# Optimization experiments

Hardware: AMD Instinct MI355X
Metric: run time of the kernel (lower is better)

## Reference

```python
import jax, jax.numpy as jnp
import numpy as np

H = 32  # hidden_size
I = 1   # input_size
O = 12  # fc output

def setup_inputs() -> dict:
    key = jax.random.key(0)
    ks = jax.random.split(key, 8)
    B, T = 4096, 512
    s_ih = 1.0 / np.sqrt(H)
    x = jax.random.normal(ks[0], (B, T, I), dtype=jnp.float32)
    w_ih = jax.random.uniform(ks[1], (3 * H, I), minval=-s_ih, maxval=s_ih, dtype=jnp.float32)
    w_hh = jax.random.uniform(ks[2], (3 * H, H), minval=-s_ih, maxval=s_ih, dtype=jnp.float32)
    b_ih = jax.random.uniform(ks[3], (3 * H,), minval=-s_ih, maxval=s_ih, dtype=jnp.float32)
    b_hh = jax.random.uniform(ks[4], (3 * H,), minval=-s_ih, maxval=s_ih, dtype=jnp.float32)
    s_fc = 1.0 / np.sqrt(H)
    fc_w = jax.random.uniform(ks[5], (O, H), minval=-s_fc, maxval=s_fc, dtype=jnp.float32)
    fc_b = jax.random.uniform(ks[6], (O,), minval=-s_fc, maxval=s_fc, dtype=jnp.float32)
    return {"x": x, "w_ih": w_ih, "w_hh": w_hh, "b_ih": b_ih, "b_hh": b_hh, "fc_w": fc_w, "fc_b": fc_b}

def _gru_last_hidden(x, w_ih, w_hh, b_ih, b_hh):
    # x: [B, T, I]. Precompute input projections for all timesteps: [B, T, 3H]
    gi = jnp.einsum('bti,gi->btg', x, w_ih) + b_ih
    gi = jnp.swapaxes(gi, 0, 1)  # [T, B, 3H] for scan over time
    B = x.shape[0]
    h0 = jnp.zeros((B, H), dtype=x.dtype)

    def step(h, gi_t):
        gh = h @ w_hh.T + b_hh  # [B, 3H]
        i_r, i_z, i_n = jnp.split(gi_t, 3, axis=-1)
        h_r, h_z, h_n = jnp.split(gh, 3, axis=-1)
        r = jax.nn.sigmoid(i_r + h_r)
        z = jax.nn.sigmoid(i_z + h_z)
        n = jnp.tanh(i_n + r * h_n)
        h_new = (1.0 - z) * n + z * h
        return h_new, None

    h_last, _ = jax.lax.scan(step, h0, gi)
    return h_last  # [B, H]

def reference(x, w_ih, w_hh, b_ih, b_hh, fc_w, fc_b):
    h_last = _gru_last_hidden(x, w_ih, w_hh, b_ih, b_hh)
    return h_last @ fc_w.T + fc_b  # [B, 12]
```

## Files before the change

### kernel.cpp

```cpp
#include <hip/hip_runtime.h>


namespace {

typedef _Float16 f16;
typedef _Float16 f16x8 __attribute__((ext_vector_type(8)));
typedef float    f32x4 __attribute__((ext_vector_type(4)));

constexpr int kT = 512;
constexpr float kL2E = 1.4426950408889634f;

__device__ __forceinline__ float fast_exp2(float a) {
#if __has_builtin(__builtin_amdgcn_exp2f)
    return __builtin_amdgcn_exp2f(a);
#else
    return exp2f(a);
#endif
}
__device__ __forceinline__ float fast_rcp(float a) {
#if __has_builtin(__builtin_amdgcn_rcpf)
    return __builtin_amdgcn_rcpf(a);
#else
    return 1.0f / a;
#endif
}

union B128 {
    int   w[4];
    f16x8 v;
};

__device__ __forceinline__ float sel4(const f32x4& a, bool b0, bool b1) {
    const float x01 = b0 ? a[1] : a[0];
    const float x23 = b0 ? a[3] : a[2];
    return b1 ? x23 : x01;
}

__global__ __launch_bounds__(64)
__attribute__((amdgpu_waves_per_eu(1, 1)))
void gru_k32s2(
    const float* __restrict__ x,
    const float* __restrict__ w_ih,
    const float* __restrict__ w_hh,
    const float* __restrict__ b_ih,
    const float* __restrict__ b_hh,
    const float* __restrict__ fc_w,
    const float* __restrict__ fc_b,
    float* __restrict__ out)
{
    __shared__ float hf[4 * 33];

    const int lane = threadIdx.x;
    const int c    = lane & 15;
    const int lg   = lane >> 4;
    const int q    = c >> 2;
    const int j    = c & 3;
    const int blk  = blockIdx.x;

    f16x8 wA[3][2];
#pragma unroll
    for (int g = 0; g < 3; ++g) {
        const float s = (g < 2) ? -kL2E : 2.0f * kL2E;
#pragma unroll
        for (int hh = 0; hh < 2; ++hh) {
            f16x8 f;
#pragma unroll
            for (int i = 0; i < 8; ++i) {
                const int k = ((i & 1) << 4) | (lg << 2) | (i >> 1);
                f[i] = (f16)(s * w_hh[(g * 32 + hh * 16 + c) * 32 + k]);
            }
            wA[g][hh] = f;
        }
    }

    f32x4 biasC[3][2];
#pragma unroll
    for (int hh = 0; hh < 2; ++hh)
#pragma unroll
        for (int v = 0; v < 4; ++v) {
            const int u = hh * 16 + 4 * lg + v;
            biasC[0][hh][v] = -kL2E * (b_ih[u] + b_hh[u]);
            biasC[1][hh][v] = -kL2E * (b_ih[u + 32] + b_hh[u + 32]);
            biasC[2][hh][v] = 2.0f * kL2E * b_hh[u + 64];
        }

    float cwr[2], cwz[2], cwn[2], cbn[2];
#pragma unroll
    for (int hh = 0; hh < 2; ++hh) {
        const int u = hh * 16 + 4 * lg + q;
        cwr[hh] = -kL2E * w_ih[u];
        cwz[hh] = -kL2E * w_ih[u + 32];
        cwn[hh] = 2.0f * kL2E * w_ih[u + 64];
        cbn[hh] = 2.0f * kL2E * b_ih[u + 64];
    }
    const bool b0 = (q & 1) != 0;
    const bool b1 = (q & 2) != 0;

    float hlo = 0.0f, hhi = 0.0f;
    B128 B;
    B.w[0] = 0; B.w[1] = 0; B.w[2] = 0; B.w[3] = 0;

    const float4* xrow = reinterpret_cast<const float4*>(
        x + ((size_t)blk * 4 + j) * kT);
    float4 xcur = xrow[0];

    for (int t0 = 0; t0 < kT; t0 += 4) {
        const int nq = (t0 + 4 < kT) ? (t0 >> 2) + 1 : (t0 >> 2);
        float4 xnext = xrow[nq];

#pragma unroll
        for (int tt = 0; tt < 4; ++tt) {
            const float xt = (tt == 0) ? xcur.x : (tt == 1) ? xcur.y
                           : (tt == 2) ? xcur.z : xcur.w;

            f32x4 aR[2], aZ[2], aN[2];
#pragma unroll
            for (int hh = 0; hh < 2; ++hh) {
                aR[hh] = __builtin_amdgcn_mfma_f32_16x16x32_f16(wA[0][hh], B.v, biasC[0][hh], 0, 0, 0);
                aZ[hh] = __builtin_amdgcn_mfma_f32_16x16x32_f16(wA[1][hh], B.v, biasC[1][hh], 0, 0, 0);
                aN[hh] = __builtin_amdgcn_mfma_f32_16x16x32_f16(wA[2][hh], B.v, biasC[2][hh], 0, 0, 0);
            }

#pragma unroll
            for (int hh = 0; hh < 2; ++hh) {
                const float pr = sel4(aR[hh], b0, b1);
                const float pz = sel4(aZ[hh], b0, b1);
                const float pn = sel4(aN[hh], b0, b1);
                const float ar  = fmaf(xt, cwr[hh], pr);
                const float az  = fmaf(xt, cwz[hh], pz);
                const float inn = fmaf(xt, cwn[hh], cbn[hh]);
                const float sr = 1.0f + fast_exp2(ar);
                const float sz = 1.0f + fast_exp2(az);
                const float ip = fast_rcp(sr * sz);
                const float r  = ip * sz;
                const float z  = ip * sr;
                const float n = fmaf(-2.0f,
                    fast_rcp(1.0f + fast_exp2(fmaf(r, pn, inn))), 1.0f);
                if (hh == 0) hlo = fmaf(z, hlo - n, n);
                else         hhi = fmaf(z, hhi - n, n);
            }

            const int pk = __builtin_bit_cast(int,
                __builtin_amdgcn_cvt_pkrtz(hlo, hhi));
            B.w[0] = __builtin_amdgcn_ds_swizzle(pk, 0x0013);
            B.w[1] = __builtin_amdgcn_ds_swizzle(pk, 0x0093);
            B.w[2] = __builtin_amdgcn_ds_swizzle(pk, 0x0113);
            B.w[3] = __builtin_amdgcn_ds_swizzle(pk, 0x0193);
        }
        xcur = xnext;
    }

    hf[j * 33 + 4 * lg + q]      = hlo;
    hf[j * 33 + 16 + 4 * lg + q] = hhi;
    __syncthreads();
    if (lane < 48) {
        const int row = lane / 12, o = lane % 12;
        float acc = fc_b[o];
#pragma unroll
        for (int k = 0; k < 32; ++k)
            acc = fmaf(fc_w[o * 32 + k], hf[row * 33 + k], acc);
        out[((size_t)blk * 4 + row) * 12 + o] = acc;
    }
}

}

extern "C" void kernel_launch(void* const* d_in, const int* in_sizes, int n_in,
                              void* d_out, int out_size, void* d_ws, size_t ws_size,
                              hipStream_t stream) {
    const float* x    = (const float*)d_in[0];
    const float* w_ih = (const float*)d_in[1];
    const float* w_hh = (const float*)d_in[2];
    const float* b_ih = (const float*)d_in[3];
    const float* b_hh = (const float*)d_in[4];
    const float* fc_w = (const float*)d_in[5];
    const float* fc_b = (const float*)d_in[6];
    float* out = (float*)d_out;

    dim3 grid(1024);
    dim3 block(64);
    gru_k32s2<<<grid, block, 0, stream>>>(x, w_ih, w_hh, b_ih, b_hh, fc_w, fc_b, out);
}
```

Before: 120.4 us.

## Split GRU hidden units across two waves with LDS exchange per step

Each block now runs two wavefronts, and each one owns 16 of the 32 hidden units, so a wave issues 3 MFMAs per step instead of 6. The new hidden state is exchanged through double-buffered shared memory with a __syncthreads every timestep, replacing the in-wave ds_swizzle broadcast. This is meant to halve the serial per-wave work on the recurrent critical path. In exchange it adds an LDS store, a block barrier and an LDS load to every one of the 512 dependent steps.

```diff
diff --git a/kernel.cpp b/kernel.cpp
--- a/kernel.cpp
+++ b/kernel.cpp
@@ -25,20 +25,15 @@
 #endif
 }
 
-union B128 {
-    int   w[4];
-    f16x8 v;
-};
-
 __device__ __forceinline__ float sel4(const f32x4& a, bool b0, bool b1) {
     const float x01 = b0 ? a[1] : a[0];
     const float x23 = b0 ? a[3] : a[2];
     return b1 ? x23 : x01;
 }
 
-__global__ __launch_bounds__(64)
-__attribute__((amdgpu_waves_per_eu(1, 1)))
-void gru_k32s2(
+__global__ __launch_bounds__(128)
+__attribute__((amdgpu_waves_per_eu(2, 2)))
+void gru_2w(
     const float* __restrict__ x,
     const float* __restrict__ w_ih,
     const float* __restrict__ w_hh,
@@ -48,57 +43,49 @@
     const float* __restrict__ fc_b,
     float* __restrict__ out)
 {
+    __shared__ f16   hbuf[2][4][32];
     __shared__ float hf[4 * 33];
 
-    const int lane = threadIdx.x;
+    const int tid  = threadIdx.x;
+    const int w    = tid >> 6;
+    const int lane = tid & 63;
     const int c    = lane & 15;
     const int lg   = lane >> 4;
     const int q    = c >> 2;
     const int j    = c & 3;
     const int blk  = blockIdx.x;
 
-    f16x8 wA[3][2];
+    f16x8 wA[3];
 #pragma unroll
     for (int g = 0; g < 3; ++g) {
         const float s = (g < 2) ? -kL2E : 2.0f * kL2E;
+        f16x8 f;
 #pragma unroll
-        for (int hh = 0; hh < 2; ++hh) {
-            f16x8 f;
-#pragma unroll
-            for (int i = 0; i < 8; ++i) {
-                const int k = ((i & 1) << 4) | (lg << 2) | (i >> 1);
-                f[i] = (f16)(s * w_hh[(g * 32 + hh * 16 + c) * 32 + k]);
-            }
-            wA[g][hh] = f;
-        }
+        for (int i = 0; i < 8; ++i)
+            f[i] = (f16)(s * w_hh[(g * 32 + w * 16 + c) * 32 + 8 * lg + i]);
+        wA[g] = f;
     }
 
-    f32x4 biasC[3][2];
+    f32x4 biasC[3];
 #pragma unroll
-    for (int hh = 0; hh < 2; ++hh)
-#pragma unroll
-        for (int v = 0; v < 4; ++v) {
-            const int u = hh * 16 + 4 * lg + v;
-            biasC[0][hh][v] = -kL2E * (b_ih[u] + b_hh[u]);
-            biasC[1][hh][v] = -kL2E * (b_ih[u + 32] + b_hh[u + 32]);
-            biasC[2][hh][v] = 2.0f * kL2E * b_hh[u + 64];
-        }
+    for (int v = 0; v < 4; ++v) {
+        const int u = w * 16 + 4 * lg + v;
+        biasC[0][v] = -kL2E * (b_ih[u] + b_hh[u]);
+        biasC[1][v] = -kL2E * (b_ih[u + 32] + b_hh[u + 32]);
+        biasC[2][v] = 2.0f * kL2E * b_hh[u + 64];
+    }
 
-    float cwr[2], cwz[2], cwn[2], cbn[2];
-#pragma unroll
-    for (int hh = 0; hh < 2; ++hh) {
-        const int u = hh * 16 + 4 * lg + q;
-        cwr[hh] = -kL2E * w_ih[u];
-        cwz[hh] = -kL2E * w_ih[u + 32];
-        cwn[hh] = 2.0f * kL2E * w_ih[u + 64];
-        cbn[hh] = 2.0f * kL2E * b_ih[u + 64];
-    }
+    const int u = w * 16 + 4 * lg + q;
+    const float cwr = -kL2E * w_ih[u];
+    const float cwz = -kL2E * w_ih[u + 32];
+    const float cwn = 2.0f * kL2E * w_ih[u + 64];
+    const float cbn = 2.0f * kL2E * b_ih[u + 64];
     const bool b0 = (q & 1) != 0;
     const bool b1 = (q & 2) != 0;
 
-    float hlo = 0.0f, hhi = 0.0f;
-    B128 B;
-    B.w[0] = 0; B.w[1] = 0; B.w[2] = 0; B.w[3] = 0;
+    float h = 0.0f;
+    f16x8 B = {(f16)0, (f16)0, (f16)0, (f16)0,
+               (f16)0, (f16)0, (f16)0, (f16)0};
 
     const float4* xrow = reinterpret_cast<const float4*>(
         x + ((size_t)blk * 4 + j) * kT);
@@ -112,49 +99,38 @@
         for (int tt = 0; tt < 4; ++tt) {
             const float xt = (tt == 0) ? xcur.x : (tt == 1) ? xcur.y
                            : (tt == 2) ? xcur.z : xcur.w;
+            const int buf = tt & 1;
 
-            f32x4 aR[2], aZ[2], aN[2];
-#pragma unroll
-            for (int hh = 0; hh < 2; ++hh) {
-                aR[hh] = __builtin_amdgcn_mfma_f32_16x16x32_f16(wA[0][hh], B.v, biasC[0][hh], 0, 0, 0);
-                aZ[hh] = __builtin_amdgcn_mfma_f32_16x16x32_f16(wA[1][hh], B.v, biasC[1][hh], 0, 0, 0);
-                aN[hh] = __builtin_amdgcn_mfma_f32_16x16x32_f16(wA[2][hh], B.v, biasC[2][hh], 0, 0, 0);
-            }
+            const f32x4 aR = __builtin_amdgcn_mfma_f32_16x16x32_f16(wA[0], B, biasC[0], 0, 0, 0);
+            const f32x4 aZ = __builtin_amdgcn_mfma_f32_16x16x32_f16(wA[1], B, biasC[1], 0, 0, 0);
+            const f32x4 aN = __builtin_amdgcn_mfma_f32_16x16x32_f16(wA[2], B, biasC[2], 0, 0, 0);
 
-#pragma unroll
-            for (int hh = 0; hh < 2; ++hh) {
-                const float pr = sel4(aR[hh], b0, b1);
-                const float pz = sel4(aZ[hh], b0, b1);
-                const float pn = sel4(aN[hh], b0, b1);
-                const float ar  = fmaf(xt, cwr[hh], pr);
-                const float az  = fmaf(xt, cwz[hh], pz);
-                const float inn = fmaf(xt, cwn[hh], cbn[hh]);
-                const float sr = 1.0f + fast_exp2(ar);
-                const float sz = 1.0f + fast_exp2(az);
-                const float ip = fast_rcp(sr * sz);
-                const float r  = ip * sz;
-                const float z  = ip * sr;
-                const float n = fmaf(-2.0f,
-                    fast_rcp(1.0f + fast_exp2(fmaf(r, pn, inn))), 1.0f);
-                if (hh == 0) hlo = fmaf(z, hlo - n, n);
-                else         hhi = fmaf(z, hhi - n, n);
-            }
+            const float pr = sel4(aR, b0, b1);
+            const float pz = sel4(aZ, b0, b1);
+            const float pn = sel4(aN, b0, b1);
+            const float ar  = fmaf(xt, cwr, pr);
+            const float az  = fmaf(xt, cwz, pz);
+            const float inn = fmaf(xt, cwn, cbn);
+            const float sr = 1.0f + fast_exp2(ar);
+            const float sz = 1.0f + fast_exp2(az);
+            const float ip = fast_rcp(sr * sz);
+            const float r  = ip * sz;
+            const float z  = ip * sr;
+            const float n = fmaf(-2.0f,
+                fast_rcp(1.0f + fast_exp2(fmaf(r, pn, inn))), 1.0f);
+            h = fmaf(z, h - n, n);
 
-            const int pk = __builtin_bit_cast(int,
-                __builtin_amdgcn_cvt_pkrtz(hlo, hhi));
-            B.w[0] = __builtin_amdgcn_ds_swizzle(pk, 0x0013);
-            B.w[1] = __builtin_amdgcn_ds_swizzle(pk, 0x0093);
-            B.w[2] = __builtin_amdgcn_ds_swizzle(pk, 0x0113);
-            B.w[3] = __builtin_amdgcn_ds_swizzle(pk, 0x0193);
+            hbuf[buf][j][u] = (f16)h;
+            __syncthreads();
+            B = *reinterpret_cast<const f16x8*>(&hbuf[buf][j][8 * lg]);
         }
         xcur = xnext;
     }
 
-    hf[j * 33 + 4 * lg + q]      = hlo;
-    hf[j * 33 + 16 + 4 * lg + q] = hhi;
+    hf[j * 33 + u] = h;
     __syncthreads();
-    if (lane < 48) {
-        const int row = lane / 12, o = lane % 12;
+    if (tid < 48) {
+        const int row = tid / 12, o = tid % 12;
         float acc = fc_b[o];
 #pragma unroll
         for (int k = 0; k < 32; ++k)
@@ -178,6 +154,6 @@
     float* out = (float*)d_out;
 
     dim3 grid(1024);
-    dim3 block(64);
-    gru_k32s2<<<grid, block, 0, stream>>>(x, w_ih, w_hh, b_ih, b_hh, fc_w, fc_b, out);
+    dim3 block(128);
+    gru_2w<<<grid, block, 0, stream>>>(x, w_ih, w_hh, b_ih, b_hh, fc_w, fc_b, out);
 }
```

Result: faster. 107.7 us, median of 2 (-10.6%).
